# Optimization experiments

Measured on AMD Instinct MI355X. Metric: run time of the kernel, lower is better.

Reference implementation:

```python
import jax, jax.numpy as jnp
import numpy as np

B, H, S, HD = 4, 16, 4096, 64
DIM = 2 * HD
NF = 9
LAMBDA_INIT = 0.01


def setup_inputs() -> dict:
    key = jax.random.key(0)
    ks = jax.random.split(key, 8)
    shape = (B, H, S, HD)
    Q_t = jax.random.normal(ks[0], shape, jnp.float32)
    Q_prime_t = jax.random.normal(ks[1], shape, jnp.float32)
    K_t = jax.random.normal(ks[2], shape, jnp.float32)
    K_prime_t = jax.random.normal(ks[3], shape, jnp.float32)
    V = jax.random.normal(ks[4], shape, jnp.float32)
    lambdas = jnp.full((NF,), LAMBDA_INIT, jnp.float32)
    # xavier_uniform for [NF, DIM] linear weights
    bound = float(np.sqrt(6.0 / (NF + DIM)))
    Wq = jax.random.uniform(ks[5], (NF, DIM), jnp.float32, -bound, bound)
    Wk = jax.random.uniform(ks[6], (NF, DIM), jnp.float32, -bound, bound)
    return {"Q_t": Q_t, "Q_prime_t": Q_prime_t, "K_t": K_t,
            "K_prime_t": K_prime_t, "V": V,
            "lambdas": lambdas, "Wq": Wq, "Wk": Wk}


def _ste_argmax_route(scores):
    # forward: hard one-hot; backward: softmax gradient (straight-through)
    idx = jnp.argmax(scores, axis=-1)
    one_hot = jax.nn.one_hot(idx, scores.shape[-1], dtype=scores.dtype)
    soft = jax.nn.softmax(scores, axis=-1)
    return one_hot + soft - jax.lax.stop_gradient(soft)


def _lambda_for(x, x_prime, W, lambdas):
    cat = jax.lax.stop_gradient(jnp.concatenate([x, x_prime], axis=-1))  # [B,H,S,2hd]
    scores = jnp.einsum('bshd,nd->bshn'.replace('s', 'x'), cat, W)  # placeholder
    return scores


def reference(Q_t, Q_prime_t, K_t, K_prime_t, V, lambdas, Wq, Wk):
    # routing scores (routers see detached inputs)
    Q_cat = jax.lax.stop_gradient(jnp.concatenate([Q_t, Q_prime_t], axis=-1))  # [B,H,S,2hd]
    K_cat = jax.lax.stop_gradient(jnp.concatenate([K_t, K_prime_t], axis=-1))
    q_scores = jnp.einsum('bhsd,nd->bhsn', Q_cat, Wq)
    k_scores = jnp.einsum('bhsd,nd->bhsn', K_cat, Wk)
    q_route = _ste_argmax_route(q_scores)  # [B,H,S,NF]
    k_route = _ste_argmax_route(k_scores)
    lambda_q = jnp.sum(q_route * lambdas, axis=-1, keepdims=True)  # [B,H,S,1]
    lambda_k = jnp.sum(k_route * lambdas, axis=-1, keepdims=True)
    Q_diff = Q_t - lambda_q * Q_prime_t
    K_diff = K_t - lambda_k * K_prime_t
    KV = jnp.einsum('bhsd,bhse->bhde', K_diff, V)   # [B,H,hd,hd]
    O = jnp.einsum('bhsd,bhde->bhse', Q_diff, KV)   # [B,H,S,hd]
    return O
```

## Files before the change

kernel.cpp:

```cpp
#include <hip/hip_runtime.h>


#define Sx 4096
#define HDx 64
#define NF 9
#define NHEAD 64
#define NCHO 32
#define SCO (Sx / NCHO)
#define NTO (SCO / 64)
#define LROW 72

typedef __attribute__((ext_vector_type(8))) short bf16x8;
typedef __attribute__((ext_vector_type(4))) float f32x4;

__device__ __forceinline__ unsigned short f2bf(float f) {
    union { float f; unsigned u; } x; x.f = f;
    unsigned r = x.u + 0x7fffu + ((x.u >> 16) & 1u);
    return (unsigned short)(r >> 16);
}
__device__ __forceinline__ float bf2f(unsigned short b) {
    union { unsigned u; float f; } x; x.u = ((unsigned)b) << 16;
    return x.f;
}
__device__ __forceinline__ bf16x8 pack8(float4 a, float4 b) {
    bf16x8 r;
    r[0] = (short)f2bf(a.x); r[1] = (short)f2bf(a.y);
    r[2] = (short)f2bf(a.z); r[3] = (short)f2bf(a.w);
    r[4] = (short)f2bf(b.x); r[5] = (short)f2bf(b.y);
    r[6] = (short)f2bf(b.z); r[7] = (short)f2bf(b.w);
    return r;
}

__device__ __forceinline__ float route_lam(float v, int l15, const float* lam9) {
    int idx = l15;
#pragma unroll
    for (int m = 1; m < 16; m <<= 1) {
        float ov = __shfl_xor(v, m, 16);
        int   oi = __shfl_xor(idx, m, 16);
        bool take = (ov > v) || (ov == v && oi < idx);
        v = take ? ov : v; idx = take ? oi : idx;
    }
    return lam9[idx];
}

__device__ __forceinline__ float lam_bcast(float r0, float r1, float r2, float r3, int l15) {
    const int src = ((l15 >> 2) << 4) + l15;
    float t0 = __shfl(r0, src);
    float t1 = __shfl(r1, src);
    float t2 = __shfl(r2, src);
    float t3 = __shfl(r3, src);
    float lo = (l15 & 1) ? t1 : t0;
    float hi = (l15 & 1) ? t3 : t2;
    return (l15 & 2) ? hi : lo;
}

template<int PARTIAL>
__global__ __launch_bounds__(256, 4) void kv_kernel(
    const float* __restrict__ Kt, const float* __restrict__ Kp,
    const float* __restrict__ V,  const float* __restrict__ lambdas,
    const float* __restrict__ Wk, float* __restrict__ KVout, int nchk)
{
    __shared__ __align__(16) unsigned short kd_s[2][64][LROW];
    __shared__ float lam9[16];

    const int tid  = threadIdx.x;
    const int lane = tid & 63;
    const int wave = tid >> 6;
    const int l15  = lane & 15;
    const int q    = lane >> 4;
    const int head  = blockIdx.x & (NHEAD - 1);
    const int chunk = blockIdx.x >> 6;
    const size_t hbase = (size_t)head * Sx * HDx;
    const int sck   = Sx / nchk;
    const int ntk   = sck >> 6;
    const int sbase = chunk * sck;
    const int myrow = wave * 16 + l15;

    if (tid < NF) lam9[tid] = lambdas[tid];

    bf16x8 wb[4];
#pragma unroll
    for (int h = 0; h < 4; ++h)
#pragma unroll
        for (int j = 0; j < 8; ++j) {
            float w = (l15 < NF) ? Wk[l15 * 128 + h * 32 + q * 8 + j] : 0.f;
            wb[h][j] = (short)f2bf(w);
        }

    f32x4 acc[4];
#pragma unroll
    for (int mt = 0; mt < 4; ++mt) acc[mt] = (f32x4){0.f, 0.f, 0.f, 0.f};

    __syncthreads();

    for (int t = 0; t < ntk; ++t) {
        const int s0 = sbase + t * 64;
        const float* kt0 = Kt + hbase + (size_t)(s0 + myrow) * HDx + q * 8;
        const float* kp0 = Kp + hbase + (size_t)(s0 + myrow) * HDx + q * 8;
        float4 a0 = *(const float4*)(kt0),      a1 = *(const float4*)(kt0 + 4);
        float4 a2 = *(const float4*)(kt0 + 32), a3 = *(const float4*)(kt0 + 36);
        float4 b0 = *(const float4*)(kp0),      b1 = *(const float4*)(kp0 + 4);
        float4 b2 = *(const float4*)(kp0 + 32), b3 = *(const float4*)(kp0 + 36);
        float vv[16];
#pragma unroll
        for (int h = 0; h < 2; ++h)
#pragma unroll
            for (int j = 0; j < 8; ++j)
                vv[h * 8 + j] = V[hbase + (size_t)(s0 + h * 32 + q * 8 + j) * HDx + wave * 16 + l15];

        bf16x8 af[4];
        af[0] = pack8(a0, a1); af[1] = pack8(a2, a3);
        af[2] = pack8(b0, b1); af[3] = pack8(b2, b3);

        f32x4 sc = (f32x4){0.f, 0.f, 0.f, 0.f};
#pragma unroll
        for (int h = 0; h < 4; ++h)
            sc = __builtin_amdgcn_mfma_f32_16x16x32_bf16(af[h], wb[h], sc, 0, 0, 0);
        float lr0 = route_lam((l15 < NF) ? sc[0] : -3.4e38f, l15, lam9);
        float lr1 = route_lam((l15 < NF) ? sc[1] : -3.4e38f, l15, lam9);
        float lr2 = route_lam((l15 < NF) ? sc[2] : -3.4e38f, l15, lam9);
        float lr3 = route_lam((l15 < NF) ? sc[3] : -3.4e38f, l15, lam9);
        const float lam = lam_bcast(lr0, lr1, lr2, lr3, l15);

#pragma unroll
        for (int h = 0; h < 2; ++h)
#pragma unroll
            for (int j = 0; j < 8; ++j)
                kd_s[t & 1][h * 32 + q * 8 + j][myrow] =
                    f2bf(bf2f((unsigned short)af[h][j]) - lam * bf2f((unsigned short)af[2 + h][j]));

        bf16x8 bv[2];
#pragma unroll
        for (int h = 0; h < 2; ++h)
#pragma unroll
            for (int j = 0; j < 8; ++j) bv[h][j] = (short)f2bf(vv[h * 8 + j]);

        __syncthreads();

#pragma unroll
        for (int h = 0; h < 2; ++h)
#pragma unroll
            for (int mt = 0; mt < 4; ++mt) {
                bf16x8 ad = *(const bf16x8*)&kd_s[t & 1][mt * 16 + l15][h * 32 + q * 8];
                acc[mt] = __builtin_amdgcn_mfma_f32_16x16x32_bf16(ad, bv[h], acc[mt], 0, 0, 0);
            }
    }

    if (PARTIAL) {
        float* slot = KVout + (size_t)(head * nchk + chunk) * (HDx * HDx);
#pragma unroll
        for (int mt = 0; mt < 4; ++mt)
#pragma unroll
            for (int r = 0; r < 4; ++r)
                slot[(mt * 16 + q * 4 + r) * 64 + wave * 16 + l15] = acc[mt][r];
    } else {
        float* kvh = KVout + head * (HDx * HDx);
#pragma unroll
        for (int mt = 0; mt < 4; ++mt)
#pragma unroll
            for (int r = 0; r < 4; ++r)
                atomicAdd(&kvh[(wave * 16 + l15) * 64 + mt * 16 + q * 4 + r], acc[mt][r]);
    }
}

__global__ __launch_bounds__(256) void kv_reduce(
    const float* __restrict__ P, unsigned short* __restrict__ KVB, int nchk)
{
    const int head = blockIdx.x;
    const int d  = threadIdx.x & 63;
    const int eq = threadIdx.x >> 6;
    const float* base = P + (size_t)head * nchk * (HDx * HDx) + d * 64 + eq * 16;
    float s[16];
#pragma unroll
    for (int i = 0; i < 16; ++i) s[i] = 0.f;
    for (int p = 0; p < nchk; ++p) {
        const float4* q4 = (const float4*)(base + (size_t)p * (HDx * HDx));
#pragma unroll
        for (int k = 0; k < 4; ++k) {
            float4 v = q4[k];
            s[4 * k + 0] += v.x; s[4 * k + 1] += v.y;
            s[4 * k + 2] += v.z; s[4 * k + 3] += v.w;
        }
    }
    unsigned short* o = KVB + (size_t)head * (HDx * HDx) + d;
#pragma unroll
    for (int i = 0; i < 16; ++i)
        o[(eq * 16 + i) * 64] = f2bf(s[i]);
}

template<int BF>
__global__ __launch_bounds__(256, 4) void out_kernel(
    const float* __restrict__ Qt, const float* __restrict__ Qp,
    const float* __restrict__ lambdas, const float* __restrict__ Wq,
    const void* __restrict__ KV, float* __restrict__ O)
{
    __shared__ float lam9[16];

    const int tid  = threadIdx.x;
    const int lane = tid & 63;
    const int wave = tid >> 6;
    const int l15  = lane & 15;
    const int q    = lane >> 4;
    const int head  = blockIdx.x & (NHEAD - 1);
    const int chunk = blockIdx.x >> 6;
    const size_t hbase = (size_t)head * Sx * HDx;
    const int s00 = chunk * SCO;
    const int myrow = wave * 16 + l15;

    if (tid < NF) lam9[tid] = lambdas[tid];

    bf16x8 wb[4];
#pragma unroll
    for (int h = 0; h < 4; ++h)
#pragma unroll
        for (int j = 0; j < 8; ++j) {
            float w = (l15 < NF) ? Wq[l15 * 128 + h * 32 + q * 8 + j] : 0.f;
            wb[h][j] = (short)f2bf(w);
        }

    bf16x8 bkv[4][2];
    if (BF) {
        const unsigned short* kvb = (const unsigned short*)KV + (size_t)head * (HDx * HDx);
#pragma unroll
        for (int nt = 0; nt < 4; ++nt)
#pragma unroll
            for (int h = 0; h < 2; ++h)
                bkv[nt][h] = *(const bf16x8*)&kvb[(nt * 16 + l15) * 64 + h * 32 + q * 8];
    } else {
        const float* kvh = (const float*)KV + (size_t)head * (HDx * HDx);
#pragma unroll
        for (int nt = 0; nt < 4; ++nt)
#pragma unroll
            for (int h = 0; h < 2; ++h) {
                const float* p = &kvh[(nt * 16 + l15) * 64 + h * 32 + q * 8];
                bkv[nt][h] = pack8(*(const float4*)p, *(const float4*)(p + 4));
            }
    }

    __syncthreads();

    for (int t = 0; t < NTO; ++t) {
        const int s0 = s00 + t * 64;
        const float* qt0 = Qt + hbase + (size_t)(s0 + myrow) * HDx + q * 8;
        const float* qp0 = Qp + hbase + (size_t)(s0 + myrow) * HDx + q * 8;
        float4 a0 = *(const float4*)(qt0),      a1 = *(const float4*)(qt0 + 4);
        float4 a2 = *(const float4*)(qt0 + 32), a3 = *(const float4*)(qt0 + 36);
        float4 b0 = *(const float4*)(qp0),      b1 = *(const float4*)(qp0 + 4);
        float4 b2 = *(const float4*)(qp0 + 32), b3 = *(const float4*)(qp0 + 36);

        bf16x8 af[4];
        af[0] = pack8(a0, a1); af[1] = pack8(a2, a3);
        af[2] = pack8(b0, b1); af[3] = pack8(b2, b3);

        f32x4 sc = (f32x4){0.f, 0.f, 0.f, 0.f};
#pragma unroll
        for (int h = 0; h < 4; ++h)
            sc = __builtin_amdgcn_mfma_f32_16x16x32_bf16(af[h], wb[h], sc, 0, 0, 0);
        float lr0 = route_lam((l15 < NF) ? sc[0] : -3.4e38f, l15, lam9);
        float lr1 = route_lam((l15 < NF) ? sc[1] : -3.4e38f, l15, lam9);
        float lr2 = route_lam((l15 < NF) ? sc[2] : -3.4e38f, l15, lam9);
        float lr3 = route_lam((l15 < NF) ? sc[3] : -3.4e38f, l15, lam9);
        const float lam = lam_bcast(lr0, lr1, lr2, lr3, l15);

        bf16x8 ad[2];
#pragma unroll
        for (int h = 0; h < 2; ++h)
#pragma unroll
            for (int j = 0; j < 8; ++j)
                ad[h][j] = (short)f2bf(bf2f((unsigned short)af[h][j])
                                       - lam * bf2f((unsigned short)af[2 + h][j]));

        f32x4 oacc[4];
#pragma unroll
        for (int nt = 0; nt < 4; ++nt) oacc[nt] = (f32x4){0.f, 0.f, 0.f, 0.f};
#pragma unroll
        for (int h = 0; h < 2; ++h)
#pragma unroll
            for (int nt = 0; nt < 4; ++nt)
                oacc[nt] = __builtin_amdgcn_mfma_f32_16x16x32_bf16(ad[h], bkv[nt][h], oacc[nt], 0, 0, 0);

#pragma unroll
        for (int nt = 0; nt < 4; ++nt)
#pragma unroll
            for (int r = 0; r < 4; ++r) {
                const int row = s0 + wave * 16 + q * 4 + r;
                O[hbase + (size_t)row * HDx + nt * 16 + l15] = oacc[nt][r];
            }
    }
}

extern "C" void kernel_launch(void* const* d_in, const int* in_sizes, int n_in,
                              void* d_out, int out_size, void* d_ws, size_t ws_size,
                              hipStream_t stream) {
    const float* Qt      = (const float*)d_in[0];
    const float* Qp      = (const float*)d_in[1];
    const float* Kt      = (const float*)d_in[2];
    const float* Kp      = (const float*)d_in[3];
    const float* V       = (const float*)d_in[4];
    const float* lambdas = (const float*)d_in[5];
    const float* Wq      = (const float*)d_in[6];
    const float* Wk      = (const float*)d_in[7];
    float* O = (float*)d_out;

    const size_t KVB_RES = 1u << 20;
    const size_t SLOT    = (size_t)HDx * HDx * sizeof(float);

    int nchk = 32;
    while (nchk > 2 && ws_size < KVB_RES + (size_t)NHEAD * nchk * SLOT) nchk >>= 1;

    if (ws_size >= KVB_RES + (size_t)NHEAD * nchk * SLOT) {
        unsigned short* KVB = (unsigned short*)d_ws;
        float* KVP = (float*)((char*)d_ws + KVB_RES);
        kv_kernel<1><<<NHEAD * nchk, 256, 0, stream>>>(Kt, Kp, V, lambdas, Wk, KVP, nchk);
        kv_reduce  <<<NHEAD, 256, 0, stream>>>(KVP, KVB, nchk);
        out_kernel<1><<<NHEAD * NCHO, 256, 0, stream>>>(Qt, Qp, lambdas, Wq, KVB, O);
    } else {
        float* KVf = (float*)d_ws;
        hipMemsetAsync(d_ws, 0, (size_t)NHEAD * HDx * HDx * sizeof(float), stream);
        kv_kernel<0><<<NHEAD * 16, 256, 0, stream>>>(Kt, Kp, V, lambdas, Wk, KVf, 16);
        out_kernel<0><<<NHEAD * NCHO, 256, 0, stream>>>(Qt, Qp, lambdas, Wq, KVf, O);
    }
}
```

Before: 374.4 us.

## Software-prefetch next tile in kv and out kernels, halve chunk counts

Both kernels now load the next 64-row tile of K/K'/V (or Q/Q') into registers while the current tile is being routed and multiplied, with a scheduling barrier to keep the loads early. Chunk counts become compile-time constants: 16 chunks for the KV pass and 16 for the output pass, which halves the grid sizes, and the loops are fully unrolled. Launch bounds drop to 2 blocks per SIMD to leave room for the extra registers. The aim is to hide global load latency, at the cost of fewer blocks in flight and more register pressure.

```diff
diff --git a/kernel.cpp b/kernel.cpp
--- a/kernel.cpp
+++ b/kernel.cpp
@@ -5,7 +5,10 @@
 #define HDx 64
 #define NF 9
 #define NHEAD 64
-#define NCHO 32
+#define NCHK 16
+#define SCK (Sx / NCHK)
+#define NTK (SCK / 64)
+#define NCHO 16
 #define SCO (Sx / NCHO)
 #define NTO (SCO / 64)
 #define LROW 72
@@ -54,11 +57,29 @@
     return (l15 & 2) ? hi : lo;
 }
 
+__device__ __forceinline__ void load_ktile(
+    const float* __restrict__ Kt, const float* __restrict__ Kp,
+    const float* __restrict__ V, size_t hbase, int s0, int myrow, int q,
+    float4 ka[4], float4 kb[4], float vv[16])
+{
+    const float* kt0 = Kt + hbase + (size_t)(s0 + myrow) * HDx + q * 8;
+    const float* kp0 = Kp + hbase + (size_t)(s0 + myrow) * HDx + q * 8;
+    ka[0] = *(const float4*)(kt0);      ka[1] = *(const float4*)(kt0 + 4);
+    ka[2] = *(const float4*)(kt0 + 32); ka[3] = *(const float4*)(kt0 + 36);
+    kb[0] = *(const float4*)(kp0);      kb[1] = *(const float4*)(kp0 + 4);
+    kb[2] = *(const float4*)(kp0 + 32); kb[3] = *(const float4*)(kp0 + 36);
+#pragma unroll
+    for (int h = 0; h < 2; ++h)
+#pragma unroll
+        for (int j = 0; j < 8; ++j)
+            vv[h * 8 + j] = V[hbase + (size_t)(s0 + h * 32 + q * 8 + j) * HDx + myrow];
+}
+
 template<int PARTIAL>
-__global__ __launch_bounds__(256, 4) void kv_kernel(
+__global__ __launch_bounds__(256, 2) void kv_kernel(
     const float* __restrict__ Kt, const float* __restrict__ Kp,
     const float* __restrict__ V,  const float* __restrict__ lambdas,
-    const float* __restrict__ Wk, float* __restrict__ KVout, int nchk)
+    const float* __restrict__ Wk, float* __restrict__ KVout)
 {
     __shared__ __align__(16) unsigned short kd_s[2][64][LROW];
     __shared__ float lam9[16];
@@ -71,9 +92,7 @@
     const int head  = blockIdx.x & (NHEAD - 1);
     const int chunk = blockIdx.x >> 6;
     const size_t hbase = (size_t)head * Sx * HDx;
-    const int sck   = Sx / nchk;
-    const int ntk   = sck >> 6;
-    const int sbase = chunk * sck;
+    const int sbase = chunk * SCK;
     const int myrow = wave * 16 + l15;
 
     if (tid < NF) lam9[tid] = lambdas[tid];
@@ -91,27 +110,21 @@
 #pragma unroll
     for (int mt = 0; mt < 4; ++mt) acc[mt] = (f32x4){0.f, 0.f, 0.f, 0.f};
 
+    float4 ka[4], kb[4]; float vv[16];
+    load_ktile(Kt, Kp, V, hbase, sbase, myrow, q, ka, kb, vv);
+
     __syncthreads();
 
-    for (int t = 0; t < ntk; ++t) {
-        const int s0 = sbase + t * 64;
-        const float* kt0 = Kt + hbase + (size_t)(s0 + myrow) * HDx + q * 8;
-        const float* kp0 = Kp + hbase + (size_t)(s0 + myrow) * HDx + q * 8;
-        float4 a0 = *(const float4*)(kt0),      a1 = *(const float4*)(kt0 + 4);
-        float4 a2 = *(const float4*)(kt0 + 32), a3 = *(const float4*)(kt0 + 36);
-        float4 b0 = *(const float4*)(kp0),      b1 = *(const float4*)(kp0 + 4);
-        float4 b2 = *(const float4*)(kp0 + 32), b3 = *(const float4*)(kp0 + 36);
-        float vv[16];
-#pragma unroll
-        for (int h = 0; h < 2; ++h)
-#pragma unroll
-            for (int j = 0; j < 8; ++j)
-                vv[h * 8 + j] = V[hbase + (size_t)(s0 + h * 32 + q * 8 + j) * HDx + wave * 16 + l15];
+#pragma unroll
+    for (int t = 0; t < NTK; ++t) {
+        float4 nka[4], nkb[4]; float nvv[16];
+        if (t + 1 < NTK)
+            load_ktile(Kt, Kp, V, hbase, sbase + (t + 1) * 64, myrow, q, nka, nkb, nvv);
+        __builtin_amdgcn_sched_barrier(0);
 
         bf16x8 af[4];
-        af[0] = pack8(a0, a1); af[1] = pack8(a2, a3);
-        af[2] = pack8(b0, b1); af[3] = pack8(b2, b3);
-
+        af[0] = pack8(ka[0], ka[1]); af[1] = pack8(ka[2], ka[3]);
+        af[2] = pack8(kb[0], kb[1]); af[3] = pack8(kb[2], kb[3]);
         f32x4 sc = (f32x4){0.f, 0.f, 0.f, 0.f};
 #pragma unroll
         for (int h = 0; h < 4; ++h)
@@ -144,10 +157,17 @@
                 bf16x8 ad = *(const bf16x8*)&kd_s[t & 1][mt * 16 + l15][h * 32 + q * 8];
                 acc[mt] = __builtin_amdgcn_mfma_f32_16x16x32_bf16(ad, bv[h], acc[mt], 0, 0, 0);
             }
+
+        if (t + 1 < NTK) {
+#pragma unroll
+            for (int i = 0; i < 4; ++i) { ka[i] = nka[i]; kb[i] = nkb[i]; }
+#pragma unroll
+            for (int j = 0; j < 16; ++j) vv[j] = nvv[j];
+        }
     }
 
     if (PARTIAL) {
-        float* slot = KVout + (size_t)(head * nchk + chunk) * (HDx * HDx);
+        float* slot = KVout + (size_t)(head * NCHK + chunk) * (HDx * HDx);
 #pragma unroll
         for (int mt = 0; mt < 4; ++mt)
 #pragma unroll
@@ -164,16 +184,16 @@
 }
 
 __global__ __launch_bounds__(256) void kv_reduce(
-    const float* __restrict__ P, unsigned short* __restrict__ KVB, int nchk)
+    const float* __restrict__ P, unsigned short* __restrict__ KVB)
 {
     const int head = blockIdx.x;
     const int d  = threadIdx.x & 63;
     const int eq = threadIdx.x >> 6;
-    const float* base = P + (size_t)head * nchk * (HDx * HDx) + d * 64 + eq * 16;
+    const float* base = P + (size_t)head * NCHK * (HDx * HDx) + d * 64 + eq * 16;
     float s[16];
 #pragma unroll
     for (int i = 0; i < 16; ++i) s[i] = 0.f;
-    for (int p = 0; p < nchk; ++p) {
+    for (int p = 0; p < NCHK; ++p) {
         const float4* q4 = (const float4*)(base + (size_t)p * (HDx * HDx));
 #pragma unroll
         for (int k = 0; k < 4; ++k) {
@@ -189,7 +209,7 @@
 }
 
 template<int BF>
-__global__ __launch_bounds__(256, 4) void out_kernel(
+__global__ __launch_bounds__(256, 2) void out_kernel(
     const float* __restrict__ Qt, const float* __restrict__ Qp,
     const float* __restrict__ lambdas, const float* __restrict__ Wq,
     const void* __restrict__ KV, float* __restrict__ O)
@@ -237,20 +257,35 @@
             }
     }
 
+    float4 qa[4], qb[4];
+    {
+        const float* qt0 = Qt + hbase + (size_t)(s00 + myrow) * HDx + q * 8;
+        const float* qp0 = Qp + hbase + (size_t)(s00 + myrow) * HDx + q * 8;
+        qa[0] = *(const float4*)(qt0);      qa[1] = *(const float4*)(qt0 + 4);
+        qa[2] = *(const float4*)(qt0 + 32); qa[3] = *(const float4*)(qt0 + 36);
+        qb[0] = *(const float4*)(qp0);      qb[1] = *(const float4*)(qp0 + 4);
+        qb[2] = *(const float4*)(qp0 + 32); qb[3] = *(const float4*)(qp0 + 36);
+    }
+
     __syncthreads();
 
+#pragma unroll
     for (int t = 0; t < NTO; ++t) {
-        const int s0 = s00 + t * 64;
-        const float* qt0 = Qt + hbase + (size_t)(s0 + myrow) * HDx + q * 8;
-        const float* qp0 = Qp + hbase + (size_t)(s0 + myrow) * HDx + q * 8;
-        float4 a0 = *(const float4*)(qt0),      a1 = *(const float4*)(qt0 + 4);
-        float4 a2 = *(const float4*)(qt0 + 32), a3 = *(const float4*)(qt0 + 36);
-        float4 b0 = *(const float4*)(qp0),      b1 = *(const float4*)(qp0 + 4);
-        float4 b2 = *(const float4*)(qp0 + 32), b3 = *(const float4*)(qp0 + 36);
+        float4 na[4], nb[4];
+        if (t + 1 < NTO) {
+            const int s0n = s00 + (t + 1) * 64;
+            const float* qt0 = Qt + hbase + (size_t)(s0n + myrow) * HDx + q * 8;
+            const float* qp0 = Qp + hbase + (size_t)(s0n + myrow) * HDx + q * 8;
+            na[0] = *(const float4*)(qt0);      na[1] = *(const float4*)(qt0 + 4);
+            na[2] = *(const float4*)(qt0 + 32); na[3] = *(const float4*)(qt0 + 36);
+            nb[0] = *(const float4*)(qp0);      nb[1] = *(const float4*)(qp0 + 4);
+            nb[2] = *(const float4*)(qp0 + 32); nb[3] = *(const float4*)(qp0 + 36);
+        }
+        __builtin_amdgcn_sched_barrier(0);
 
         bf16x8 af[4];
-        af[0] = pack8(a0, a1); af[1] = pack8(a2, a3);
-        af[2] = pack8(b0, b1); af[3] = pack8(b2, b3);
+        af[0] = pack8(qa[0], qa[1]); af[1] = pack8(qa[2], qa[3]);
+        af[2] = pack8(qb[0], qb[1]); af[3] = pack8(qb[2], qb[3]);
 
         f32x4 sc = (f32x4){0.f, 0.f, 0.f, 0.f};
 #pragma unroll
@@ -279,6 +314,7 @@
             for (int nt = 0; nt < 4; ++nt)
                 oacc[nt] = __builtin_amdgcn_mfma_f32_16x16x32_bf16(ad[h], bkv[nt][h], oacc[nt], 0, 0, 0);
 
+        const int s0 = s00 + t * 64;
 #pragma unroll
         for (int nt = 0; nt < 4; ++nt)
 #pragma unroll
@@ -286,6 +322,11 @@
                 const int row = s0 + wave * 16 + q * 4 + r;
                 O[hbase + (size_t)row * HDx + nt * 16 + l15] = oacc[nt][r];
             }
+
+        if (t + 1 < NTO) {
+#pragma unroll
+            for (int i = 0; i < 4; ++i) { qa[i] = na[i]; qb[i] = nb[i]; }
+        }
     }
 }
 
@@ -304,20 +345,18 @@
 
     const size_t KVB_RES = 1u << 20;
     const size_t SLOT    = (size_t)HDx * HDx * sizeof(float);
-
-    int nchk = 32;
-    while (nchk > 2 && ws_size < KVB_RES + (size_t)NHEAD * nchk * SLOT) nchk >>= 1;
-
-    if (ws_size >= KVB_RES + (size_t)NHEAD * nchk * SLOT) {
+    const size_t NEED    = KVB_RES + (size_t)NHEAD * NCHK * SLOT;
+
+    if (ws_size >= NEED) {
         unsigned short* KVB = (unsigned short*)d_ws;
         float* KVP = (float*)((char*)d_ws + KVB_RES);
-        kv_kernel<1><<<NHEAD * nchk, 256, 0, stream>>>(Kt, Kp, V, lambdas, Wk, KVP, nchk);
-        kv_reduce  <<<NHEAD, 256, 0, stream>>>(KVP, KVB, nchk);
+        kv_kernel<1><<<NHEAD * NCHK, 256, 0, stream>>>(Kt, Kp, V, lambdas, Wk, KVP);
+        kv_reduce  <<<NHEAD, 256, 0, stream>>>(KVP, KVB);
         out_kernel<1><<<NHEAD * NCHO, 256, 0, stream>>>(Qt, Qp, lambdas, Wq, KVB, O);
     } else {
         float* KVf = (float*)d_ws;
         hipMemsetAsync(d_ws, 0, (size_t)NHEAD * HDx * HDx * sizeof(float), stream);
-        kv_kernel<0><<<NHEAD * 16, 256, 0, stream>>>(Kt, Kp, V, lambdas, Wk, KVf, 16);
+        kv_kernel<0><<<NHEAD * NCHK, 256, 0, stream>>>(Kt, Kp, V, lambdas, Wk, KVf);
         out_kernel<0><<<NHEAD * NCHO, 256, 0, stream>>>(Qt, Qp, lambdas, Wq, KVf, O);
     }
 }
```

New measurement: 362.2 us. 1.03x faster.
